# Kernel tuning notes

Measured on AMD Instinct MI355X. Metric: run time of the kernel, lower is better.

Reference implementation:

```python
import jax, jax.numpy as jnp
import numpy as np

N_HEADS = 16
N_DIM = 1024
H_DIM = N_DIM // N_HEADS


def setup_inputs() -> dict:
    key = jax.random.key(0)
    ks = jax.random.split(key, 9)
    s = 1.0 / np.sqrt(N_DIM)
    x = jax.random.normal(ks[0], (4, 2048, N_DIM), dtype=jnp.float32)
    Wq = jax.random.uniform(ks[1], (N_DIM, N_DIM), jnp.float32, -s, s)
    bq = jax.random.uniform(ks[2], (N_DIM,), jnp.float32, -s, s)
    Wk = jax.random.uniform(ks[3], (N_DIM, N_DIM), jnp.float32, -s, s)
    bk = jax.random.uniform(ks[4], (N_DIM,), jnp.float32, -s, s)
    Wv = jax.random.uniform(ks[5], (N_DIM, N_DIM), jnp.float32, -s, s)
    bv = jax.random.uniform(ks[6], (N_DIM,), jnp.float32, -s, s)
    Wp = jax.random.uniform(ks[7], (N_DIM, N_DIM), jnp.float32, -s, s)
    bp = jax.random.uniform(ks[8], (N_DIM,), jnp.float32, -s, s)
    return {"x": x, "Wq": Wq, "bq": bq, "Wk": Wk, "bk": bk,
            "Wv": Wv, "bv": bv, "Wp": Wp, "bp": bp}


def _split_heads(y):
    # [b, t, (nh*hd)] -> [nh, b, t, hd]
    b, t, _ = y.shape
    return y.reshape(b, t, N_HEADS, H_DIM).transpose(2, 0, 1, 3)


def reference(x, Wq, bq, Wk, bk, Wv, bv, Wp, bp):
    q = _split_heads(x @ Wq.T + bq)
    k = _split_heads(x @ Wk.T + bk)
    v = _split_heads(x @ Wv.T + bv)
    # NOTE: original module applies NO 1/sqrt(d) scaling
    energies = jnp.einsum('hbqd,hbkd->hbqk', q, k)
    attn = jax.nn.softmax(energies, axis=-1)  # dropout disabled (eval)
    out = jnp.einsum('hbqk,hbkd->hbqd', attn, v)
    # [nh, b, t, hd] -> [b, t, nh*hd]
    b, t = out.shape[1], out.shape[2]
    out = out.transpose(1, 2, 0, 3).reshape(b, t, N_DIM)
    return out @ Wp.T + bp
```

## Files before the change

### kernel.cpp

```cpp
#include <hip/hip_runtime.h>
#include <hip/hip_bf16.h>


typedef short short8 __attribute__((ext_vector_type(8)));
typedef float float4v __attribute__((ext_vector_type(4)));

#define MFMA16(a, b, c) __builtin_amdgcn_mfma_f32_16x16x32_bf16((a), (b), (c), 0, 0, 0)
#define LOG2E 1.4426950408889634f

#define B_SZ 4
#define T_SZ 2048
#define D_SZ 1024
#define NH 16
#define HD 64
#define M_SZ (B_SZ * T_SZ)

__device__ __forceinline__ unsigned short f2bf(float f) {
  unsigned int u = __float_as_uint(f);
  u += 0x7fffu + ((u >> 16) & 1u);
  return (unsigned short)(u >> 16);
}

__device__ __forceinline__ float fexp2(float x) {
#if __has_builtin(__builtin_amdgcn_exp2f)
  return __builtin_amdgcn_exp2f(x);
#else
  return exp2f(x);
#endif
}

__device__ __forceinline__ void gl_lds16(const unsigned short* g, unsigned short* l) {
  __builtin_amdgcn_global_load_lds(
      (const __attribute__((address_space(1))) unsigned int*)g,
      (__attribute__((address_space(3))) unsigned int*)l, 16, 0, 0);
}

__global__ __launch_bounds__(256) void cvt_kernel(const float* __restrict__ in,
                                                  unsigned short* __restrict__ out,
                                                  float scale, long n) {
  long i = ((long)blockIdx.x * 256 + threadIdx.x) * 4;
  if (i >= n) return;
  float4 v = *(const float4*)(in + i);
  uint2 o;
  o.x = (unsigned)f2bf(v.x * scale) | ((unsigned)f2bf(v.y * scale) << 16);
  o.y = (unsigned)f2bf(v.z * scale) | ((unsigned)f2bf(v.w * scale) << 16);
  *(uint2*)(out + i) = o;
}

__global__ __launch_bounds__(256) void cvt_w(const float* __restrict__ w0,
                                             const float* __restrict__ w1,
                                             const float* __restrict__ w2,
                                             const float* __restrict__ w3,
                                             unsigned short* __restrict__ out, long per) {
  long i = ((long)blockIdx.x * 256 + threadIdx.x) * 4;
  int which = (int)(i / per);
  const float* src = which == 0 ? w0 : which == 1 ? w1 : which == 2 ? w2 : w3;
  float scale = which == 0 ? LOG2E : 1.0f;
  long j = i - (long)which * per;
  float4 v = *(const float4*)(src + j);
  uint2 o;
  o.x = (unsigned)f2bf(v.x * scale) | ((unsigned)f2bf(v.y * scale) << 16);
  o.y = (unsigned)f2bf(v.z * scale) | ((unsigned)f2bf(v.w * scale) << 16);
  *(uint2*)(out + i) = o;
}

__global__ __launch_bounds__(256) void cvt_bias(const float* __restrict__ b0,
                                                const float* __restrict__ b1,
                                                const float* __restrict__ b2,
                                                float* __restrict__ out) {
  int i = blockIdx.x * 256 + threadIdx.x;
  float v;
  if (i < 1024) v = b0[i] * LOG2E;
  else if (i < 2048) v = b1[i - 1024];
  else v = b2[i - 2048];
  out[i] = v;
}

__global__ __launch_bounds__(256, 3) void gemm_qkv(const unsigned short* __restrict__ A,
                                                   const unsigned short* __restrict__ W,
                                                   const float* __restrict__ bias,
                                                   unsigned short* __restrict__ Qb,
                                                   unsigned short* __restrict__ Kb,
                                                   unsigned short* __restrict__ Vt) {
  __shared__ __align__(16) unsigned short smem[17408];
  unsigned short* As = smem;
  unsigned short* Bs = smem + 8192;
  unsigned short* Ct = smem;
  const int tid = threadIdx.x;
  const int wave = tid >> 6, lane = tid & 63;
  const int q = lane >> 4, ln = lane & 15;
  const int wm = (wave >> 1) * 64, wn = (wave & 1) * 64;
  const long m0 = (long)blockIdx.y * 128;
  const long n0 = (long)blockIdx.x * 128;
  const int srow = lane >> 3, scol = (lane & 7) * 8;
  const int K = D_SZ;

  float4v acc[4][4] = {};

  for (int k0 = 0; k0 < K; k0 += 64) {
    for (int t = 0; t < 4; ++t) {
      int seg = wave * 4 + t;
      int row = seg * 8 + srow;
      gl_lds16(A + (m0 + row) * (long)K + k0 + scol, As + seg * 512);
      gl_lds16(W + (n0 + row) * (long)K + k0 + scol, Bs + seg * 512);
    }
    __syncthreads();
    for (int ks = 0; ks < 2; ++ks) {
      short8 af[4], bf[4];
      for (int i = 0; i < 4; ++i)
        af[i] = *(const short8*)(As + (wm + i * 16 + ln) * 64 + ks * 32 + q * 8);
      for (int j = 0; j < 4; ++j)
        bf[j] = *(const short8*)(Bs + (wn + j * 16 + ln) * 64 + ks * 32 + q * 8);
      for (int i = 0; i < 4; ++i)
        for (int j = 0; j < 4; ++j)
          acc[i][j] = MFMA16(af[i], bf[j], acc[i][j]);
    }
    __syncthreads();
  }

  if ((int)n0 < 2048) {
    unsigned short* dst = (int)n0 < 1024 ? Qb : Kb;
    int coff = (int)n0 < 1024 ? 0 : 1024;
    for (int i = 0; i < 4; ++i) {
      long rowb = m0 + wm + i * 16 + q * 4;
      for (int j = 0; j < 4; ++j) {
        long col = n0 + wn + j * 16 + ln;
        float bv = bias[col];
        for (int r = 0; r < 4; ++r)
          dst[(rowb + r) * (long)D_SZ + col - coff] = f2bf(acc[i][j][r] + bv);
      }
    }
  } else {
    for (int i = 0; i < 4; ++i)
      for (int j = 0; j < 4; ++j) {
        int col_l = wn + j * 16 + ln;
        float bv = bias[n0 + col_l];
        __hip_bfloat162 lo =
            __float22bfloat162_rn(make_float2(acc[i][j][0] + bv, acc[i][j][1] + bv));
        __hip_bfloat162 hi =
            __float22bfloat162_rn(make_float2(acc[i][j][2] + bv, acc[i][j][3] + bv));
        uint2 w;
        w.x = *(unsigned*)&lo;
        w.y = *(unsigned*)&hi;
        *(uint2*)(Ct + col_l * 136 + wm + i * 16 + q * 4) = w;
      }
    __syncthreads();
    for (int it = 0; it < 8; ++it) {
      int idx = tid + it * 256;
      int c = idx >> 4, rb = idx & 15;
      uint4 v = *(const uint4*)(Ct + c * 136 + rb * 8);
      *(uint4*)(Vt + (n0 - 2048 + c) * (long)M_SZ + m0 + rb * 8) = v;
    }
  }
}

__global__ __launch_bounds__(256, 3) void gemm_proj(const unsigned short* __restrict__ A,
                                                    const unsigned short* __restrict__ W,
                                                    const float* __restrict__ bias,
                                                    float* __restrict__ Cf) {
  __shared__ __align__(16) unsigned short As[128 * 64];
  __shared__ __align__(16) unsigned short Bs[128 * 64];
  const int tid = threadIdx.x;
  const int wave = tid >> 6, lane = tid & 63;
  const int q = lane >> 4, ln = lane & 15;
  const int wm = (wave >> 1) * 64, wn = (wave & 1) * 64;
  const long m0 = (long)blockIdx.y * 128;
  const long n0 = (long)blockIdx.x * 128;
  const int srow = lane >> 3, scol = (lane & 7) * 8;
  const int K = D_SZ;

  float4v acc[4][4] = {};
  for (int k0 = 0; k0 < K; k0 += 64) {
    for (int t = 0; t < 4; ++t) {
      int seg = wave * 4 + t;
      int row = seg * 8 + srow;
      gl_lds16(A + (m0 + row) * (long)K + k0 + scol, As + seg * 512);
      gl_lds16(W + (n0 + row) * (long)K + k0 + scol, Bs + seg * 512);
    }
    __syncthreads();
    for (int ks = 0; ks < 2; ++ks) {
      short8 af[4], bf[4];
      for (int i = 0; i < 4; ++i)
        af[i] = *(const short8*)(As + (wm + i * 16 + ln) * 64 + ks * 32 + q * 8);
      for (int j = 0; j < 4; ++j)
        bf[j] = *(const short8*)(Bs + (wn + j * 16 + ln) * 64 + ks * 32 + q * 8);
      for (int i = 0; i < 4; ++i)
        for (int j = 0; j < 4; ++j)
          acc[i][j] = MFMA16(af[i], bf[j], acc[i][j]);
    }
    __syncthreads();
  }
  for (int i = 0; i < 4; ++i) {
    long rowb = m0 + wm + i * 16 + q * 4;
    for (int j = 0; j < 4; ++j) {
      long col = n0 + wn + j * 16 + ln;
      float bv = bias[col];
      for (int r = 0; r < 4; ++r)
        Cf[(rowb + r) * (long)D_SZ + col] = acc[i][j][r] + bv;
    }
  }
}

__global__ __launch_bounds__(512, 4) void attn_kernel(const unsigned short* __restrict__ Qb,
                                                      const unsigned short* __restrict__ Kb,
                                                      const unsigned short* __restrict__ Vt,
                                                      unsigned short* __restrict__ Ob) {
  __shared__ __align__(16) unsigned short KV[16384];
  __shared__ __align__(16) unsigned short Pp[10240];

  const int tid = threadIdx.x;
  const int wave = tid >> 6, lane = tid & 63;
  const int q = lane >> 4, ln = lane & 15;
  const int l7 = lane & 7, l3 = lane >> 3;
  const int qt = blockIdx.x, h = blockIdx.y, b = blockIdx.z;

  const long baseQ = ((long)b * T_SZ + qt * 256) * D_SZ + h * HD;
  const long baseK = (long)b * T_SZ * D_SZ + h * HD;
  const long baseV = (long)h * HD * M_SZ + (long)b * T_SZ;
  const int cs = ((l7 ^ l3) * 8);

  short8 qf[2][2];
  for (int i = 0; i < 2; ++i)
    for (int ks = 0; ks < 2; ++ks)
      qf[i][ks] = *(const short8*)(Qb + baseQ + (long)(wave * 32 + i * 16 + ln) * D_SZ +
                                   ks * 32 + q * 8);

  float4v o[2][4] = {};
  float lp[2] = {};
  unsigned short* Ppw = Pp + wave * (32 * 40);
  const int swz = (ln & 7) * 8;

#define STAGE(kt_, base_)                                                                \
  {                                                                                      \
    int row = wave * 8 + l3;                                                             \
    gl_lds16(Kb + baseK + (long)((kt_)*64 + row) * D_SZ + cs, (base_) + wave * 512);     \
    gl_lds16(Vt + baseV + (long)row * M_SZ + (kt_)*64 + cs, (base_) + 4096 + wave * 512);\
  }

  STAGE(0, KV)

  for (int kt = 0; kt < 32; ++kt) {
    unsigned short* cur = KV + (kt & 1) * 8192;
    unsigned short* nxt = KV + ((kt & 1) ^ 1) * 8192;
    __syncthreads();
    if (kt < 31) { STAGE(kt + 1, nxt) }

    short8 kf[4][2];
    for (int c = 0; c < 4; ++c)
      for (int ks = 0; ks < 2; ++ks)
        kf[c][ks] = *(const short8*)(cur + (c * 16 + ln) * 64 + ((ks * 32 + q * 8) ^ swz));
    float4v s[4][2];
    for (int c = 0; c < 4; ++c)
      for (int i = 0; i < 2; ++i) {
        float4v z = {};
        z = MFMA16(kf[c][0], qf[i][0], z);
        z = MFMA16(kf[c][1], qf[i][1], z);
        s[c][i] = z;
      }

    for (int ks = 0; ks < 2; ++ks) {
      for (int i = 0; i < 2; ++i)
        for (int cl = 0; cl < 2; ++cl) {
          int c = 2 * ks + cl;
          float p0 = fexp2(s[c][i][0]);
          float p1 = fexp2(s[c][i][1]);
          float p2 = fexp2(s[c][i][2]);
          float p3 = fexp2(s[c][i][3]);
          lp[i] += (p0 + p1) + (p2 + p3);
          __hip_bfloat162 lo = __float22bfloat162_rn(make_float2(p0, p1));
          __hip_bfloat162 hi = __float22bfloat162_rn(make_float2(p2, p3));
          uint2 w;
          w.x = *(unsigned*)&lo;
          w.y = *(unsigned*)&hi;
          *(uint2*)(Ppw + (i * 16 + ln) * 40 + cl * 16 + q * 4) = w;
        }
      short8 vf[4];
      for (int j = 0; j < 4; ++j)
        vf[j] = *(const short8*)(cur + 4096 + (j * 16 + ln) * 64 + ((ks * 32 + q * 8) ^ swz));
      short8 pf[2];
      for (int i = 0; i < 2; ++i)
        pf[i] = *(const short8*)(Ppw + (i * 16 + ln) * 40 + q * 8);
      for (int i = 0; i < 2; ++i)
        for (int j = 0; j < 4; ++j)
          o[i][j] = MFMA16(pf[i], vf[j], o[i][j]);
    }
  }

  for (int i = 0; i < 2; ++i) {
    float l = lp[i];
    l += __shfl_xor(l, 16, 64);
    l += __shfl_xor(l, 32, 64);
    float inv = 1.f / l;
    for (int r = 0; r < 4; ++r) {
      int src = (lane & 48) | (q * 4 + r);
      float invr = __shfl(inv, src, 64);
      int row = qt * 256 + wave * 32 + i * 16 + q * 4 + r;
      long base = ((long)b * T_SZ + row) * D_SZ + h * HD;
      for (int j = 0; j < 4; ++j)
        Ob[base + j * 16 + ln] = f2bf(o[i][j][r] * invr);
    }
  }
#undef STAGE
}

extern "C" void kernel_launch(void* const* d_in, const int* in_sizes, int n_in,
                              void* d_out, int out_size, void* d_ws, size_t ws_size,
                              hipStream_t stream) {
  const float* x = (const float*)d_in[0];
  const float* Wq = (const float*)d_in[1];
  const float* bq = (const float*)d_in[2];
  const float* Wk = (const float*)d_in[3];
  const float* bk = (const float*)d_in[4];
  const float* Wv = (const float*)d_in[5];
  const float* bv = (const float*)d_in[6];
  const float* Wp = (const float*)d_in[7];
  const float* bp = (const float*)d_in[8];
  float* out = (float*)d_out;

  const long MX = (long)M_SZ * D_SZ;
  const long MW = (long)D_SZ * D_SZ;
  unsigned short* ws = (unsigned short*)d_ws;
  unsigned short* xb = ws;
  unsigned short* Wcat = xb + MX;
  float* bcat = (float*)(Wcat + 4 * MW);
  unsigned short* Qb = (unsigned short*)(bcat + 3072);
  unsigned short* Kb = Qb + MX;
  unsigned short* Vtb = Kb + MX;
  unsigned short* Ob = Vtb + MX;

  cvt_kernel<<<(int)(MX / 1024), 256, 0, stream>>>(x, xb, 1.0f, MX);
  cvt_w<<<(int)(4 * MW / 1024), 256, 0, stream>>>(Wq, Wk, Wv, Wp, Wcat, MW);
  cvt_bias<<<12, 256, 0, stream>>>(bq, bk, bv, bcat);

  dim3 gq(3072 / 128, M_SZ / 128);
  gemm_qkv<<<gq, 256, 0, stream>>>(xb, Wcat, bcat, Qb, Kb, Vtb);

  dim3 ag(T_SZ / 256, NH, B_SZ);
  attn_kernel<<<ag, 512, 0, stream>>>(Qb, Kb, Vtb, Ob);

  dim3 gp(D_SZ / 128, M_SZ / 128);
  gemm_proj<<<gp, 256, 0, stream>>>(Ob, Wcat + 3 * MW, bp, out);
}
```

Baseline: 277.8 us.

## Merge conversion kernels and halve attention query tile per block

Replaces the three fp32-to-bf16 conversion launches with one combined kernel that dispatches on block index, removing two launches. The attention kernel now handles 128 query rows per block (16 per wave) instead of 256, doubling the grid and halving per-wave registers and LDS for P. This trades lower K/V reuse per block for higher occupancy and more blocks. It also wraps the MFMA sections in s_setprio to favour matrix issue across waves.

```diff
diff --git a/kernel.cpp b/kernel.cpp
--- a/kernel.cpp
+++ b/kernel.cpp
@@ -14,6 +14,7 @@
 #define NH 16
 #define HD 64
 #define M_SZ (B_SZ * T_SZ)
+#define MW_SZ (D_SZ * D_SZ)
 
 __device__ __forceinline__ unsigned short f2bf(float f) {
   unsigned int u = __float_as_uint(f);
@@ -35,45 +36,49 @@
       (__attribute__((address_space(3))) unsigned int*)l, 16, 0, 0);
 }
 
-__global__ __launch_bounds__(256) void cvt_kernel(const float* __restrict__ in,
-                                                  unsigned short* __restrict__ out,
-                                                  float scale, long n) {
-  long i = ((long)blockIdx.x * 256 + threadIdx.x) * 4;
-  if (i >= n) return;
-  float4 v = *(const float4*)(in + i);
-  uint2 o;
-  o.x = (unsigned)f2bf(v.x * scale) | ((unsigned)f2bf(v.y * scale) << 16);
-  o.y = (unsigned)f2bf(v.z * scale) | ((unsigned)f2bf(v.w * scale) << 16);
-  *(uint2*)(out + i) = o;
-}
-
-__global__ __launch_bounds__(256) void cvt_w(const float* __restrict__ w0,
-                                             const float* __restrict__ w1,
-                                             const float* __restrict__ w2,
-                                             const float* __restrict__ w3,
-                                             unsigned short* __restrict__ out, long per) {
-  long i = ((long)blockIdx.x * 256 + threadIdx.x) * 4;
-  int which = (int)(i / per);
-  const float* src = which == 0 ? w0 : which == 1 ? w1 : which == 2 ? w2 : w3;
-  float scale = which == 0 ? LOG2E : 1.0f;
-  long j = i - (long)which * per;
-  float4 v = *(const float4*)(src + j);
-  uint2 o;
-  o.x = (unsigned)f2bf(v.x * scale) | ((unsigned)f2bf(v.y * scale) << 16);
-  o.y = (unsigned)f2bf(v.z * scale) | ((unsigned)f2bf(v.w * scale) << 16);
-  *(uint2*)(out + i) = o;
-}
-
-__global__ __launch_bounds__(256) void cvt_bias(const float* __restrict__ b0,
-                                                const float* __restrict__ b1,
-                                                const float* __restrict__ b2,
-                                                float* __restrict__ out) {
-  int i = blockIdx.x * 256 + threadIdx.x;
-  float v;
-  if (i < 1024) v = b0[i] * LOG2E;
-  else if (i < 2048) v = b1[i - 1024];
-  else v = b2[i - 2048];
-  out[i] = v;
+__global__ __launch_bounds__(256) void cvt_all(const float* __restrict__ x,
+                                               const float* __restrict__ w0,
+                                               const float* __restrict__ w1,
+                                               const float* __restrict__ w2,
+                                               const float* __restrict__ w3,
+                                               const float* __restrict__ b0,
+                                               const float* __restrict__ b1,
+                                               const float* __restrict__ b2,
+                                               unsigned short* __restrict__ xb,
+                                               unsigned short* __restrict__ wout,
+                                               float* __restrict__ bout) {
+  const long blk = blockIdx.x;
+  if (blk < 8192) {
+    long i = (blk * 256 + threadIdx.x) * 4;
+    float4 v = *(const float4*)(x + i);
+    uint2 o;
+    o.x = (unsigned)f2bf(v.x) | ((unsigned)f2bf(v.y) << 16);
+    o.y = (unsigned)f2bf(v.z) | ((unsigned)f2bf(v.w) << 16);
+    *(uint2*)(xb + i) = o;
+  } else if (blk < 12288) {
+    long i = ((blk - 8192) * 256 + threadIdx.x) * 4;
+    int which = (int)(i >> 20);
+    const float* src = which == 0 ? w0 : which == 1 ? w1 : which == 2 ? w2 : w3;
+    float scale = which == 0 ? LOG2E : 1.0f;
+    long j = i - (long)which * MW_SZ;
+    float4 v = *(const float4*)(src + j);
+    uint2 o;
+    o.x = (unsigned)f2bf(v.x * scale) | ((unsigned)f2bf(v.y * scale) << 16);
+    o.y = (unsigned)f2bf(v.z * scale) | ((unsigned)f2bf(v.w * scale) << 16);
+    *(uint2*)(wout + i) = o;
+  } else {
+    int i = (int)((blk - 12288) * 256 + threadIdx.x) * 4;
+    float4 v;
+    if (i < 1024) {
+      v = *(const float4*)(b0 + i);
+      v.x *= LOG2E; v.y *= LOG2E; v.z *= LOG2E; v.w *= LOG2E;
+    } else if (i < 2048) {
+      v = *(const float4*)(b1 + (i - 1024));
+    } else {
+      v = *(const float4*)(b2 + (i - 2048));
+    }
+    *(float4*)(bout + i) = v;
+  }
 }
 
 __global__ __launch_bounds__(256, 3) void gemm_qkv(const unsigned short* __restrict__ A,
@@ -206,7 +211,7 @@
                                                       const unsigned short* __restrict__ Vt,
                                                       unsigned short* __restrict__ Ob) {
   __shared__ __align__(16) unsigned short KV[16384];
-  __shared__ __align__(16) unsigned short Pp[10240];
+  __shared__ __align__(16) unsigned short Pp[5120];
 
   const int tid = threadIdx.x;
   const int wave = tid >> 6, lane = tid & 63;
@@ -214,20 +219,18 @@
   const int l7 = lane & 7, l3 = lane >> 3;
   const int qt = blockIdx.x, h = blockIdx.y, b = blockIdx.z;
 
-  const long baseQ = ((long)b * T_SZ + qt * 256) * D_SZ + h * HD;
+  const long baseQ = ((long)b * T_SZ + qt * 128) * D_SZ + h * HD;
   const long baseK = (long)b * T_SZ * D_SZ + h * HD;
   const long baseV = (long)h * HD * M_SZ + (long)b * T_SZ;
   const int cs = ((l7 ^ l3) * 8);
 
-  short8 qf[2][2];
-  for (int i = 0; i < 2; ++i)
-    for (int ks = 0; ks < 2; ++ks)
-      qf[i][ks] = *(const short8*)(Qb + baseQ + (long)(wave * 32 + i * 16 + ln) * D_SZ +
-                                   ks * 32 + q * 8);
-
-  float4v o[2][4] = {};
-  float lp[2] = {};
-  unsigned short* Ppw = Pp + wave * (32 * 40);
+  short8 qf[2];
+  for (int ks = 0; ks < 2; ++ks)
+    qf[ks] = *(const short8*)(Qb + baseQ + (long)(wave * 16 + ln) * D_SZ + ks * 32 + q * 8);
+
+  float4v o[4] = {};
+  float lp = 0.f;
+  unsigned short* Ppw = Pp + wave * (16 * 40);
   const int swz = (ln & 7) * 8;
 
 #define STAGE(kt_, base_)                                                                \
@@ -249,55 +252,54 @@
     for (int c = 0; c < 4; ++c)
       for (int ks = 0; ks < 2; ++ks)
         kf[c][ks] = *(const short8*)(cur + (c * 16 + ln) * 64 + ((ks * 32 + q * 8) ^ swz));
-    float4v s[4][2];
-    for (int c = 0; c < 4; ++c)
-      for (int i = 0; i < 2; ++i) {
-        float4v z = {};
-        z = MFMA16(kf[c][0], qf[i][0], z);
-        z = MFMA16(kf[c][1], qf[i][1], z);
-        s[c][i] = z;
+    float4v s[4];
+    __builtin_amdgcn_s_setprio(1);
+    for (int c = 0; c < 4; ++c) {
+      float4v z = {};
+      z = MFMA16(kf[c][0], qf[0], z);
+      z = MFMA16(kf[c][1], qf[1], z);
+      s[c] = z;
+    }
+    __builtin_amdgcn_s_setprio(0);
+
+    for (int ks = 0; ks < 2; ++ks) {
+      for (int cl = 0; cl < 2; ++cl) {
+        int c = 2 * ks + cl;
+        float p0 = fexp2(s[c][0]);
+        float p1 = fexp2(s[c][1]);
+        float p2 = fexp2(s[c][2]);
+        float p3 = fexp2(s[c][3]);
+        lp += (p0 + p1) + (p2 + p3);
+        __hip_bfloat162 lo = __float22bfloat162_rn(make_float2(p0, p1));
+        __hip_bfloat162 hi = __float22bfloat162_rn(make_float2(p2, p3));
+        uint2 w;
+        w.x = *(unsigned*)&lo;
+        w.y = *(unsigned*)&hi;
+        *(uint2*)(Ppw + ln * 40 + cl * 16 + q * 4) = w;
       }
-
-    for (int ks = 0; ks < 2; ++ks) {
-      for (int i = 0; i < 2; ++i)
-        for (int cl = 0; cl < 2; ++cl) {
-          int c = 2 * ks + cl;
-          float p0 = fexp2(s[c][i][0]);
-          float p1 = fexp2(s[c][i][1]);
-          float p2 = fexp2(s[c][i][2]);
-          float p3 = fexp2(s[c][i][3]);
-          lp[i] += (p0 + p1) + (p2 + p3);
-          __hip_bfloat162 lo = __float22bfloat162_rn(make_float2(p0, p1));
-          __hip_bfloat162 hi = __float22bfloat162_rn(make_float2(p2, p3));
-          uint2 w;
-          w.x = *(unsigned*)&lo;
-          w.y = *(unsigned*)&hi;
-          *(uint2*)(Ppw + (i * 16 + ln) * 40 + cl * 16 + q * 4) = w;
-        }
       short8 vf[4];
       for (int j = 0; j < 4; ++j)
         vf[j] = *(const short8*)(cur + 4096 + (j * 16 + ln) * 64 + ((ks * 32 + q * 8) ^ swz));
-      short8 pf[2];
-      for (int i = 0; i < 2; ++i)
-        pf[i] = *(const short8*)(Ppw + (i * 16 + ln) * 40 + q * 8);
-      for (int i = 0; i < 2; ++i)
-        for (int j = 0; j < 4; ++j)
-          o[i][j] = MFMA16(pf[i], vf[j], o[i][j]);
-    }
-  }
-
-  for (int i = 0; i < 2; ++i) {
-    float l = lp[i];
+      short8 pf = *(const short8*)(Ppw + ln * 40 + q * 8);
+      __builtin_amdgcn_s_setprio(1);
+      for (int j = 0; j < 4; ++j)
+        o[j] = MFMA16(pf, vf[j], o[j]);
+      __builtin_amdgcn_s_setprio(0);
+    }
+  }
+
+  {
+    float l = lp;
     l += __shfl_xor(l, 16, 64);
     l += __shfl_xor(l, 32, 64);
     float inv = 1.f / l;
     for (int r = 0; r < 4; ++r) {
       int src = (lane & 48) | (q * 4 + r);
       float invr = __shfl(inv, src, 64);
-      int row = qt * 256 + wave * 32 + i * 16 + q * 4 + r;
+      int row = qt * 128 + wave * 16 + q * 4 + r;
       long base = ((long)b * T_SZ + row) * D_SZ + h * HD;
       for (int j = 0; j < 4; ++j)
-        Ob[base + j * 16 + ln] = f2bf(o[i][j][r] * invr);
+        Ob[base + j * 16 + ln] = f2bf(o[j][r] * invr);
     }
   }
 #undef STAGE
@@ -318,7 +320,7 @@
   float* out = (float*)d_out;
 
   const long MX = (long)M_SZ * D_SZ;
-  const long MW = (long)D_SZ * D_SZ;
+  const long MW = (long)MW_SZ;
   unsigned short* ws = (unsigned short*)d_ws;
   unsigned short* xb = ws;
   unsigned short* Wcat = xb + MX;
@@ -328,14 +330,12 @@
   unsigned short* Vtb = Kb + MX;
   unsigned short* Ob = Vtb + MX;
 
-  cvt_kernel<<<(int)(MX / 1024), 256, 0, stream>>>(x, xb, 1.0f, MX);
-  cvt_w<<<(int)(4 * MW / 1024), 256, 0, stream>>>(Wq, Wk, Wv, Wp, Wcat, MW);
-  cvt_bias<<<12, 256, 0, stream>>>(bq, bk, bv, bcat);
+  cvt_all<<<12291, 256, 0, stream>>>(x, Wq, Wk, Wv, Wp, bq, bk, bv, xb, Wcat, bcat);
 
   dim3 gq(3072 / 128, M_SZ / 128);
   gemm_qkv<<<gq, 256, 0, stream>>>(xb, Wcat, bcat, Qb, Kb, Vtb);
 
-  dim3 ag(T_SZ / 256, NH, B_SZ);
+  dim3 ag(T_SZ / 128, NH, B_SZ);
   attn_kernel<<<ag, 512, 0, stream>>>(Qb, Kb, Vtb, Ob);
 
   dim3 gp(D_SZ / 128, M_SZ / 128);
```

Result: no change. 282.7 us (+1.7%).
